# Kernel tuning notes

Measured on AMD Instinct MI355X. Metric: run time of the kernel, lower is better.

Reference implementation:

```python
import jax, jax.numpy as jnp
import numpy as np

N = 100000
E = 1600000
IN_C = 128
OUT_C = 128
EPS = 1e-12  # F.normalize eps


def setup_inputs() -> dict:
    key = jax.random.key(0)
    ks = jax.random.split(key, 8)
    glorot = lambda k, fi, fo: jax.random.uniform(k, (fo, fi), jnp.float32, -1.0, 1.0) * np.sqrt(1.0 / fi)
    return {
        "x": jax.random.normal(ks[0], (N, IN_C), jnp.float32),
        "edge_index": jax.random.randint(ks[1], (2, E), 0, N, jnp.int64),
        "W_l1": glorot(ks[2], IN_C, OUT_C),
        "b_l1": jnp.zeros((OUT_C,), jnp.float32),
        "W_r1": glorot(ks[3], IN_C, OUT_C),
        "W_l2": glorot(ks[4], OUT_C, OUT_C),
        "b_l2": jnp.zeros((OUT_C,), jnp.float32),
        "W_r2": glorot(ks[5], OUT_C, OUT_C),
    }


def _sage_conv(x, src, dst, W_l, b_l, W_r):
    # mean aggregation of source-node features into destination nodes
    deg = jax.ops.segment_sum(jnp.ones((src.shape[0],), x.dtype), dst, num_segments=N)
    agg = jax.ops.segment_sum(x[src], dst, num_segments=N)  # [N, C] scatter-add of gathered features
    agg = agg / jnp.maximum(deg, 1.0)[:, None]
    out = agg @ W_l.T + b_l + x @ W_r.T
    # L2 normalize (F.normalize, p=2, eps=1e-12)
    nrm = jnp.linalg.norm(out, axis=-1, keepdims=True)
    return out / jnp.maximum(nrm, EPS)


def reference(x, edge_index, W_l1, b_l1, W_r1, W_l2, b_l2, W_r2):
    src, dst = edge_index[0], edge_index[1]
    h = _sage_conv(x, src, dst, W_l1, b_l1, W_r1)
    h = _sage_conv(h, src, dst, W_l2, b_l2, W_r2)
    return h
```

## Files before the change

### kernel.cpp

```cpp
#include <hip/hip_runtime.h>
#include <hip/hip_bf16.h>


#define BCAP 16384

typedef __attribute__((ext_vector_type(8))) short bf16x8;
typedef __attribute__((ext_vector_type(4))) float f32x4;

__device__ __forceinline__ ushort f2bf(float f) {
    uint u = __float_as_uint(f);
    uint r = (u + 0x7FFFu + ((u >> 16) & 1u)) >> 16;
    return (ushort)r;
}
__device__ __forceinline__ float bflo(uint u) { return __uint_as_float(u << 16); }
__device__ __forceinline__ float bfhi(uint u) { return __uint_as_float(u & 0xFFFF0000u); }

__global__ void detect_kernel(const int* __restrict__ ei, int* __restrict__ flag) {
    if (threadIdx.x == 0 && blockIdx.x == 0) {
        int z = 1;
        for (int j = 0; j < 64; ++j)
            if (ei[2 * j + 1] != 0) { z = 0; break; }
        *flag = z;
    }
}

__device__ __forceinline__ int load_idx(const void* ei, int is64, size_t i) {
    return is64 ? (int)((const long long*)ei)[i] : ((const int*)ei)[i];
}

__global__ __launch_bounds__(256) void bin_scatter_kernel(
    const void* __restrict__ ei, const int* __restrict__ flagp,
    int* __restrict__ bcursor, uint* __restrict__ pairbuf, int E, int ntiles) {
    __shared__ int cnt[256], pos[256];
    const int tid = threadIdx.x;
    const int is64 = *flagp;
    for (int tile = blockIdx.x; tile < ntiles; tile += gridDim.x) {
        const int base = tile * 2048;
        cnt[tid] = 0;
        __syncthreads();
        int eb[8];
        uint ep[8];
#pragma unroll
        for (int j = 0; j < 8; ++j) {
            const int i = base + tid * 8 + j;
            if (i < E) {
                const int s = load_idx(ei, is64, (size_t)i);
                const int d = load_idx(ei, is64, (size_t)E + i);
                eb[j] = d >> 9;
                ep[j] = ((uint)(d & 511) << 17) | (uint)s;
                atomicAdd(&cnt[eb[j]], 1);
            } else {
                eb[j] = -1;
            }
        }
        __syncthreads();
        pos[tid] = atomicAdd(&bcursor[tid], cnt[tid]);
        __syncthreads();
#pragma unroll
        for (int j = 0; j < 8; ++j) {
            if (eb[j] >= 0) {
                const int p = atomicAdd(&pos[eb[j]], 1);
                if (p < BCAP) pairbuf[(size_t)eb[j] * BCAP + p] = ep[j];
            }
        }
    }
}

__global__ void bucket_scan_kernel(const int* __restrict__ bcount,
                                   int* __restrict__ bbase,
                                   int* __restrict__ rs, int N) {
    __shared__ int wt[4];
    const int tid = threadIdx.x, lane = tid & 63, wid = tid >> 6;
    const int v = bcount[tid];
    int incl = v;
    for (int d = 1; d < 64; d <<= 1) {
        int up = __shfl_up(incl, d, 64);
        if (lane >= d) incl += up;
    }
    if (lane == 63) wt[wid] = incl;
    __syncthreads();
    int woff = 0;
    for (int w = 0; w < wid; ++w) woff += wt[w];
    bbase[tid] = woff + incl - v;
    if (tid == 255) rs[N] = woff + incl;
}

__global__ __launch_bounds__(256) void bucket_degscan_kernel(
    const uint* __restrict__ pairbuf, const int* __restrict__ bcount,
    const int* __restrict__ bbase,
    int* __restrict__ rs, float* __restrict__ invd, int N) {
    __shared__ int dg[512];
    __shared__ int wt[4];
    const int tid = threadIdx.x, lane = tid & 63, wid = tid >> 6, wg = blockIdx.x;
    dg[tid] = 0;
    dg[tid + 256] = 0;
    __syncthreads();
    const int s = wg * BCAP, e = s + bcount[wg];
    for (int i = s + tid; i < e; i += 256)
        atomicAdd(&dg[pairbuf[i] >> 17], 1);
    __syncthreads();
    const int d0 = dg[2 * tid], d1 = dg[2 * tid + 1];
    const int v = d0 + d1;
    int incl = v;
    for (int d = 1; d < 64; d <<= 1) {
        int up = __shfl_up(incl, d, 64);
        if (lane >= d) incl += up;
    }
    if (lane == 63) wt[wid] = incl;
    __syncthreads();
    int woff = 0;
    for (int w = 0; w < wid; ++w) woff += wt[w];
    const int excl = woff + incl - v + bbase[wg];
    const int node = wg * 512 + 2 * tid;
    if (node < N) {
        rs[node] = excl;
        invd[node] = 1.0f / (float)(d0 > 1 ? d0 : 1);
    }
    if (node + 1 < N) {
        rs[node + 1] = excl + d0;
        invd[node + 1] = 1.0f / (float)(d1 > 1 ? d1 : 1);
    }
}

__global__ __launch_bounds__(256) void bucket_fill_kernel(
    const uint* __restrict__ pairbuf, const int* __restrict__ bcount,
    const int* __restrict__ rs, int* __restrict__ csr, int N) {
    __shared__ int cur[512];
    const int tid = threadIdx.x, wg = blockIdx.x;
#pragma unroll
    for (int t = tid; t < 512; t += 256) {
        const int node = wg * 512 + t;
        cur[t] = (node < N) ? rs[node] : 0;
    }
    __syncthreads();
    const int s = wg * BCAP, e = s + bcount[wg];
    for (int i = s + tid; i < e; i += 256) {
        const uint p = pairbuf[i];
        const int pos = atomicAdd(&cur[p >> 17], 1);
        csr[pos] = (int)(p & 0x1FFFFu);
    }
}

__global__ void pack_w_kernel(const float* __restrict__ Wl1, const float* __restrict__ Wr1,
                              const float* __restrict__ Wl2, const float* __restrict__ Wr2,
                              ushort* __restrict__ Wp) {
    const int gtid = blockIdx.x * 256 + threadIdx.x;
    if (gtid >= 8192) return;
    const int layer = gtid >> 12;
    const int c16   = gtid & 4095;
    const int s     = c16 >> 10;
    const int t     = (c16 >> 6) & 15;
    const int lane  = c16 & 63;
    const int c     = t * 16 + (lane & 15);
    const int kbase = s * 32 + (lane >> 4) * 8;
    const float* Wl = layer ? Wl2 : Wl1;
    const float* Wr = layer ? Wr2 : Wr1;
    const float* src = (c < 128) ? (Wl + c * 128 + kbase) : (Wr + (c - 128) * 128 + kbase);
    ushort* dst = Wp + (size_t)layer * 32768 + (size_t)c16 * 8;
#pragma unroll
    for (int j = 0; j < 8; ++j) dst[j] = f2bf(src[j]);
}

template <int AF32>
__global__ __launch_bounds__(256) void sage_mfma_gemm(
    const void* __restrict__ Av, const ushort* __restrict__ Wp,
    unsigned char* __restrict__ ylq, float* __restrict__ scales,
    ushort* __restrict__ yr, int n) {
    __shared__ ushort Wlds[16384];
    const int h = blockIdx.x & 1;
    const int mt = blockIdx.x >> 1;
    for (int i = threadIdx.x; i < 2048; i += 256) {
        const int e = i >> 6, l = i & 63;
        const int ge = (e >> 3) * 16 + h * 8 + (e & 7);
        *(bf16x8*)&Wlds[(size_t)i * 8] = *(const bf16x8*)&Wp[(size_t)(ge * 64 + l) * 8];
    }
    __syncthreads();

    const int wid = threadIdx.x >> 6, lane = threadIdx.x & 63;
    const int koff = (lane >> 4) * 8;
    const int rsub = lane & 15;

    bf16x8 a_cur[4];
    {
        int arow = mt * 64 + wid * 16 + rsub;
        if (arow >= n) arow = 0;
        if (AF32) {
            const float* ap = (const float*)Av + ((size_t)arow << 7) + koff;
#pragma unroll
            for (int s = 0; s < 4; ++s) {
                const float4 f0 = *(const float4*)(ap + s * 32);
                const float4 f1 = *(const float4*)(ap + s * 32 + 4);
                bf16x8 rr;
                rr[0] = (short)f2bf(f0.x); rr[1] = (short)f2bf(f0.y);
                rr[2] = (short)f2bf(f0.z); rr[3] = (short)f2bf(f0.w);
                rr[4] = (short)f2bf(f1.x); rr[5] = (short)f2bf(f1.y);
                rr[6] = (short)f2bf(f1.z); rr[7] = (short)f2bf(f1.w);
                a_cur[s] = rr;
            }
        } else {
            const ushort* ap = (const ushort*)Av + ((size_t)arow << 7) + koff;
#pragma unroll
            for (int s = 0; s < 4; ++s) a_cur[s] = *(const bf16x8*)(ap + s * 32);
        }
    }

    f32x4 acc[8];
    const f32x4 zero = {0.f, 0.f, 0.f, 0.f};
#pragma unroll
    for (int t = 0; t < 8; ++t) acc[t] = zero;

#pragma unroll
    for (int s = 0; s < 4; ++s) {
        const bf16x8 as = a_cur[s];
#pragma unroll
        for (int t = 0; t < 8; ++t) {
            const bf16x8 b = *(const bf16x8*)&Wlds[(size_t)((s * 8 + t) * 64 + lane) * 8];
            acc[t] = __builtin_amdgcn_mfma_f32_16x16x32_bf16(as, b, acc[t], 0, 0, 0);
        }
    }

    const int rowb = mt * 64 + wid * 16 + (lane >> 4) * 4;

    if (h == 0) {
        float mrow[4], invq[4];
#pragma unroll
        for (int rr = 0; rr < 4; ++rr) {
            float m = 0.f;
#pragma unroll
            for (int t = 0; t < 8; ++t) m = fmaxf(m, fabsf(acc[t][rr]));
            m = fmaxf(m, __shfl_xor(m, 1, 64));
            m = fmaxf(m, __shfl_xor(m, 2, 64));
            m = fmaxf(m, __shfl_xor(m, 4, 64));
            m = fmaxf(m, __shfl_xor(m, 8, 64));
            mrow[rr] = m;
            invq[rr] = 127.0f / fmaxf(m, 1e-20f);
        }
        if (rsub == 0) {
#pragma unroll
            for (int rr = 0; rr < 4; ++rr)
                if (rowb + rr < n) scales[rowb + rr] = mrow[rr] * (1.0f / 127.0f);
        }
#pragma unroll
        for (int t = 0; t < 8; ++t) {
            const int col = t * 16 + rsub;
#pragma unroll
            for (int rr = 0; rr < 4; ++rr) {
                const int row = rowb + rr;
                if (row < n) {
                    const int qv = __float2int_rn(acc[t][rr] * invq[rr]) + 128;
                    ylq[((size_t)row << 7) + col] = (unsigned char)qv;
                }
            }
        }
    } else {
#pragma unroll
        for (int t = 0; t < 8; ++t) {
            const int col = t * 16 + rsub;
#pragma unroll
            for (int rr = 0; rr < 4; ++rr) {
                const int row = rowb + rr;
                if (row < n) yr[((size_t)row << 7) + col] = f2bf(acc[t][rr]);
            }
        }
    }
}

template <int OUTF32>
__global__ __launch_bounds__(256) void aggregate_norm_kernel(
    const unsigned char* __restrict__ ylq, const float* __restrict__ scales,
    const ushort* __restrict__ yr, const float* __restrict__ bias,
    const int* __restrict__ csr, const int* __restrict__ rs,
    const float* __restrict__ invd, void* __restrict__ outp, int n) {
    const int wid = threadIdx.x >> 6, lane = threadIdx.x & 63;
    const int g = lane >> 4, t = lane & 15;
    const int node = blockIdx.x * 16 + wid * 4 + g;
    if (node >= n) return;
    const int s = rs[node], e = rs[node + 1];

    float ax[8];
#pragma unroll
    for (int j = 0; j < 8; ++j) ax[j] = 0.f;
    float sumS = 0.f;

    auto acc_row = [&](uint2 u, float sc) {
        sumS += sc;
        ax[0] = fmaf((float)(u.x & 0xffu),         sc, ax[0]);
        ax[1] = fmaf((float)((u.x >> 8) & 0xffu),  sc, ax[1]);
        ax[2] = fmaf((float)((u.x >> 16) & 0xffu), sc, ax[2]);
        ax[3] = fmaf((float)(u.x >> 24),           sc, ax[3]);
        ax[4] = fmaf((float)(u.y & 0xffu),         sc, ax[4]);
        ax[5] = fmaf((float)((u.y >> 8) & 0xffu),  sc, ax[5]);
        ax[6] = fmaf((float)((u.y >> 16) & 0xffu), sc, ax[6]);
        ax[7] = fmaf((float)(u.y >> 24),           sc, ax[7]);
    };

    int q = s;
    while (q < e && (q & 3)) {
        const int c = csr[q++];
        acc_row(*(const uint2*)(ylq + ((size_t)c << 7) + 8 * t), scales[c]);
    }
    for (; q + 4 <= e; q += 4) {
        const int4 c4 = *(const int4*)(csr + q);
        const float s0 = scales[c4.x], s1 = scales[c4.y];
        const float s2 = scales[c4.z], s3 = scales[c4.w];
        const uint2 u0 = *(const uint2*)(ylq + ((size_t)c4.x << 7) + 8 * t);
        const uint2 u1 = *(const uint2*)(ylq + ((size_t)c4.y << 7) + 8 * t);
        const uint2 u2 = *(const uint2*)(ylq + ((size_t)c4.z << 7) + 8 * t);
        const uint2 u3 = *(const uint2*)(ylq + ((size_t)c4.w << 7) + 8 * t);
        acc_row(u0, s0); acc_row(u1, s1); acc_row(u2, s2); acc_row(u3, s3);
    }
    for (; q < e; ++q) {
        const int c = csr[q];
        acc_row(*(const uint2*)(ylq + ((size_t)c << 7) + 8 * t), scales[c]);
    }

    const float iv = invd[node];
    const float base = -128.0f * sumS;
    const uint4 ur = *(const uint4*)(yr + ((size_t)node << 7) + 8 * t);
    const float4 b0 = *(const float4*)(bias + 8 * t);
    const float4 b1 = *(const float4*)(bias + 8 * t + 4);
    float v[8];
    v[0] = fmaf(ax[0] + base, iv, bflo(ur.x) + b0.x);
    v[1] = fmaf(ax[1] + base, iv, bfhi(ur.x) + b0.y);
    v[2] = fmaf(ax[2] + base, iv, bflo(ur.y) + b0.z);
    v[3] = fmaf(ax[3] + base, iv, bfhi(ur.y) + b0.w);
    v[4] = fmaf(ax[4] + base, iv, bflo(ur.z) + b1.x);
    v[5] = fmaf(ax[5] + base, iv, bfhi(ur.z) + b1.y);
    v[6] = fmaf(ax[6] + base, iv, bflo(ur.w) + b1.z);
    v[7] = fmaf(ax[7] + base, iv, bfhi(ur.w) + b1.w);

    float ss = 0.f;
#pragma unroll
    for (int j = 0; j < 8; ++j) ss = fmaf(v[j], v[j], ss);
    ss += __shfl_xor(ss, 1, 64);
    ss += __shfl_xor(ss, 2, 64);
    ss += __shfl_xor(ss, 4, 64);
    ss += __shfl_xor(ss, 8, 64);
    const float sc = 1.0f / fmaxf(sqrtf(ss), 1e-12f);

    if (OUTF32) {
        float4 o0 = {v[0] * sc, v[1] * sc, v[2] * sc, v[3] * sc};
        float4 o1 = {v[4] * sc, v[5] * sc, v[6] * sc, v[7] * sc};
        ((float4*)outp)[((size_t)node << 5) + 2 * t]     = o0;
        ((float4*)outp)[((size_t)node << 5) + 2 * t + 1] = o1;
    } else {
        uint4 o;
        o.x = (uint)f2bf(v[0] * sc) | ((uint)f2bf(v[1] * sc) << 16);
        o.y = (uint)f2bf(v[2] * sc) | ((uint)f2bf(v[3] * sc) << 16);
        o.z = (uint)f2bf(v[4] * sc) | ((uint)f2bf(v[5] * sc) << 16);
        o.w = (uint)f2bf(v[6] * sc) | ((uint)f2bf(v[7] * sc) << 16);
        ((uint4*)outp)[((size_t)node << 4) + t] = o;
    }
}

extern "C" void kernel_launch(void* const* d_in, const int* in_sizes, int n_in,
                              void* d_out, int out_size, void* d_ws, size_t ws_size,
                              hipStream_t stream) {
    const float* x   = (const float*)d_in[0];
    const void*  ei  = d_in[1];
    const float* Wl1 = (const float*)d_in[2];
    const float* bl1 = (const float*)d_in[3];
    const float* Wr1 = (const float*)d_in[4];
    const float* Wl2 = (const float*)d_in[5];
    const float* bl2 = (const float*)d_in[6];
    const float* Wr2 = (const float*)d_in[7];
    float* out = (float*)d_out;

    const int N = in_sizes[0] / 128;
    const int E = in_sizes[1] / 2;

    char* wsb = (char*)d_ws;
    size_t off = 0;
    auto alloc = [&](size_t bytes) -> void* {
        void* p = (void*)(wsb + off);
        off += bytes;
        off = (off + 255) & ~(size_t)255;
        return p;
    };

    int*    rs      = (int*)alloc(4 * (size_t)(N + 1));
    float*  invd    = (float*)alloc(4 * (size_t)N);
    float*  scales  = (float*)alloc(4 * (size_t)N);
    int*    flag    = (int*)alloc(256);
    int*    bcursor = (int*)alloc(4 * 256);
    int*    bbase   = (int*)alloc(4 * 256);
    int*    csr     = (int*)alloc(4 * (size_t)E);
    ushort* h1      = (ushort*)alloc((size_t)N * 128 * 2);
    unsigned char* ylq = (unsigned char*)alloc((size_t)N * 128);
    ushort* yr      = (ushort*)alloc((size_t)N * 128 * 2);
    ushort* Wp      = (ushort*)alloc(2 * 32768 * 2);
    uint*   pairbuf = (uint*)yr;

    const int ab = (N + 15) / 16;
    const int mtiles = (N + 63) / 64;
    const int ntiles = (E + 2047) / 2048;

    detect_kernel<<<1, 64, 0, stream>>>((const int*)ei, flag);
    hipMemsetAsync(bcursor, 0, 4 * 256, stream);
    bin_scatter_kernel<<<512, 256, 0, stream>>>(ei, flag, bcursor, pairbuf, E, ntiles);
    bucket_scan_kernel<<<1, 256, 0, stream>>>(bcursor, bbase, rs, N);
    bucket_degscan_kernel<<<256, 256, 0, stream>>>(pairbuf, bcursor, bbase, rs, invd, N);
    bucket_fill_kernel<<<256, 256, 0, stream>>>(pairbuf, bcursor, rs, csr, N);

    pack_w_kernel<<<32, 256, 0, stream>>>(Wl1, Wr1, Wl2, Wr2, Wp);

    sage_mfma_gemm<1><<<2 * mtiles, 256, 0, stream>>>(x, Wp, ylq, scales, yr, N);
    aggregate_norm_kernel<0><<<ab, 256, 0, stream>>>(ylq, scales, yr, bl1, csr, rs, invd, h1, N);

    sage_mfma_gemm<0><<<2 * mtiles, 256, 0, stream>>>(h1, Wp + 32768, ylq, scales, yr, N);
    aggregate_norm_kernel<1><<<ab, 256, 0, stream>>>(ylq, scales, yr, bl2, csr, rs, invd, out, N);
}
```

Measured before the change: 208.1 us.

## Quantize root projection to int8 and fuse CSR degree-scan with fill

```diff
diff --git a/kernel.cpp b/kernel.cpp
--- a/kernel.cpp
+++ b/kernel.cpp
@@ -85,11 +85,12 @@
     if (tid == 255) rs[N] = woff + incl;
 }
 
-__global__ __launch_bounds__(256) void bucket_degscan_kernel(
+__global__ __launch_bounds__(256) void bucket_build_kernel(
     const uint* __restrict__ pairbuf, const int* __restrict__ bcount,
     const int* __restrict__ bbase,
-    int* __restrict__ rs, float* __restrict__ invd, int N) {
+    int* __restrict__ rs, float* __restrict__ invd, int* __restrict__ csr, int N) {
     __shared__ int dg[512];
+    __shared__ int cur[512];
     __shared__ int wt[4];
     const int tid = threadIdx.x, lane = tid & 63, wid = tid >> 6, wg = blockIdx.x;
     dg[tid] = 0;
@@ -120,20 +121,9 @@
         rs[node + 1] = excl + d0;
         invd[node + 1] = 1.0f / (float)(d1 > 1 ? d1 : 1);
     }
-}
-
-__global__ __launch_bounds__(256) void bucket_fill_kernel(
-    const uint* __restrict__ pairbuf, const int* __restrict__ bcount,
-    const int* __restrict__ rs, int* __restrict__ csr, int N) {
-    __shared__ int cur[512];
-    const int tid = threadIdx.x, wg = blockIdx.x;
-#pragma unroll
-    for (int t = tid; t < 512; t += 256) {
-        const int node = wg * 512 + t;
-        cur[t] = (node < N) ? rs[node] : 0;
-    }
-    __syncthreads();
-    const int s = wg * BCAP, e = s + bcount[wg];
+    cur[2 * tid] = excl;
+    cur[2 * tid + 1] = excl + d0;
+    __syncthreads();
     for (int i = s + tid; i < e; i += 256) {
         const uint p = pairbuf[i];
         const int pos = atomicAdd(&cur[p >> 17], 1);
@@ -165,7 +155,7 @@
 __global__ __launch_bounds__(256) void sage_mfma_gemm(
     const void* __restrict__ Av, const ushort* __restrict__ Wp,
     unsigned char* __restrict__ ylq, float* __restrict__ scales,
-    ushort* __restrict__ yr, int n) {
+    unsigned char* __restrict__ yrq, float* __restrict__ scales_r, int n) {
     __shared__ ushort Wlds[16384];
     const int h = blockIdx.x & 1;
     const int mt = blockIdx.x >> 1;
@@ -220,46 +210,36 @@
     }
 
     const int rowb = mt * 64 + wid * 16 + (lane >> 4) * 4;
-
-    if (h == 0) {
-        float mrow[4], invq[4];
+    unsigned char* dq = h ? yrq : ylq;
+    float* ds = h ? scales_r : scales;
+
+    float mrow[4], invq[4];
+#pragma unroll
+    for (int rr = 0; rr < 4; ++rr) {
+        float m = 0.f;
+#pragma unroll
+        for (int t = 0; t < 8; ++t) m = fmaxf(m, fabsf(acc[t][rr]));
+        m = fmaxf(m, __shfl_xor(m, 1, 64));
+        m = fmaxf(m, __shfl_xor(m, 2, 64));
+        m = fmaxf(m, __shfl_xor(m, 4, 64));
+        m = fmaxf(m, __shfl_xor(m, 8, 64));
+        mrow[rr] = m;
+        invq[rr] = 127.0f / fmaxf(m, 1e-20f);
+    }
+    if (rsub == 0) {
+#pragma unroll
+        for (int rr = 0; rr < 4; ++rr)
+            if (rowb + rr < n) ds[rowb + rr] = mrow[rr] * (1.0f / 127.0f);
+    }
+#pragma unroll
+    for (int t = 0; t < 8; ++t) {
+        const int col = t * 16 + rsub;
 #pragma unroll
         for (int rr = 0; rr < 4; ++rr) {
-            float m = 0.f;
-#pragma unroll
-            for (int t = 0; t < 8; ++t) m = fmaxf(m, fabsf(acc[t][rr]));
-            m = fmaxf(m, __shfl_xor(m, 1, 64));
-            m = fmaxf(m, __shfl_xor(m, 2, 64));
-            m = fmaxf(m, __shfl_xor(m, 4, 64));
-            m = fmaxf(m, __shfl_xor(m, 8, 64));
-            mrow[rr] = m;
-            invq[rr] = 127.0f / fmaxf(m, 1e-20f);
-        }
-        if (rsub == 0) {
-#pragma unroll
-            for (int rr = 0; rr < 4; ++rr)
-                if (rowb + rr < n) scales[rowb + rr] = mrow[rr] * (1.0f / 127.0f);
-        }
-#pragma unroll
-        for (int t = 0; t < 8; ++t) {
-            const int col = t * 16 + rsub;
-#pragma unroll
-            for (int rr = 0; rr < 4; ++rr) {
-                const int row = rowb + rr;
-                if (row < n) {
-                    const int qv = __float2int_rn(acc[t][rr] * invq[rr]) + 128;
-                    ylq[((size_t)row << 7) + col] = (unsigned char)qv;
-                }
-            }
-        }
-    } else {
-#pragma unroll
-        for (int t = 0; t < 8; ++t) {
-            const int col = t * 16 + rsub;
-#pragma unroll
-            for (int rr = 0; rr < 4; ++rr) {
-                const int row = rowb + rr;
-                if (row < n) yr[((size_t)row << 7) + col] = f2bf(acc[t][rr]);
+            const int row = rowb + rr;
+            if (row < n) {
+                const int qv = __float2int_rn(acc[t][rr] * invq[rr]) + 128;
+                dq[((size_t)row << 7) + col] = (unsigned char)qv;
             }
         }
     }
@@ -268,9 +248,10 @@
 template <int OUTF32>
 __global__ __launch_bounds__(256) void aggregate_norm_kernel(
     const unsigned char* __restrict__ ylq, const float* __restrict__ scales,
-    const ushort* __restrict__ yr, const float* __restrict__ bias,
-    const int* __restrict__ csr, const int* __restrict__ rs,
-    const float* __restrict__ invd, void* __restrict__ outp, int n) {
+    const unsigned char* __restrict__ yrq, const float* __restrict__ scales_r,
+    const float* __restrict__ bias, const int* __restrict__ csr,
+    const int* __restrict__ rs, const float* __restrict__ invd,
+    void* __restrict__ outp, int n) {
     const int wid = threadIdx.x >> 6, lane = threadIdx.x & 63;
     const int g = lane >> 4, t = lane & 15;
     const int node = blockIdx.x * 16 + wid * 4 + g;
@@ -316,18 +297,28 @@
 
     const float iv = invd[node];
     const float base = -128.0f * sumS;
-    const uint4 ur = *(const uint4*)(yr + ((size_t)node << 7) + 8 * t);
+    const float sr = scales_r[node];
+    const uint2 ur = *(const uint2*)(yrq + ((size_t)node << 7) + 8 * t);
     const float4 b0 = *(const float4*)(bias + 8 * t);
     const float4 b1 = *(const float4*)(bias + 8 * t + 4);
+    float yv[8];
+    yv[0] = ((float)(ur.x & 0xffu)         - 128.0f) * sr;
+    yv[1] = ((float)((ur.x >> 8) & 0xffu)  - 128.0f) * sr;
+    yv[2] = ((float)((ur.x >> 16) & 0xffu) - 128.0f) * sr;
+    yv[3] = ((float)(ur.x >> 24)           - 128.0f) * sr;
+    yv[4] = ((float)(ur.y & 0xffu)         - 128.0f) * sr;
+    yv[5] = ((float)((ur.y >> 8) & 0xffu)  - 128.0f) * sr;
+    yv[6] = ((float)((ur.y >> 16) & 0xffu) - 128.0f) * sr;
+    yv[7] = ((float)(ur.y >> 24)           - 128.0f) * sr;
     float v[8];
-    v[0] = fmaf(ax[0] + base, iv, bflo(ur.x) + b0.x);
-    v[1] = fmaf(ax[1] + base, iv, bfhi(ur.x) + b0.y);
-    v[2] = fmaf(ax[2] + base, iv, bflo(ur.y) + b0.z);
-    v[3] = fmaf(ax[3] + base, iv, bfhi(ur.y) + b0.w);
-    v[4] = fmaf(ax[4] + base, iv, bflo(ur.z) + b1.x);
-    v[5] = fmaf(ax[5] + base, iv, bfhi(ur.z) + b1.y);
-    v[6] = fmaf(ax[6] + base, iv, bflo(ur.w) + b1.z);
-    v[7] = fmaf(ax[7] + base, iv, bfhi(ur.w) + b1.w);
+    v[0] = fmaf(ax[0] + base, iv, yv[0] + b0.x);
+    v[1] = fmaf(ax[1] + base, iv, yv[1] + b0.y);
+    v[2] = fmaf(ax[2] + base, iv, yv[2] + b0.z);
+    v[3] = fmaf(ax[3] + base, iv, yv[3] + b0.w);
+    v[4] = fmaf(ax[4] + base, iv, yv[4] + b1.x);
+    v[5] = fmaf(ax[5] + base, iv, yv[5] + b1.y);
+    v[6] = fmaf(ax[6] + base, iv, yv[6] + b1.z);
+    v[7] = fmaf(ax[7] + base, iv, yv[7] + b1.w);
 
     float ss = 0.f;
 #pragma unroll
@@ -378,18 +369,19 @@
         return p;
     };
 
-    int*    rs      = (int*)alloc(4 * (size_t)(N + 1));
-    float*  invd    = (float*)alloc(4 * (size_t)N);
-    float*  scales  = (float*)alloc(4 * (size_t)N);
-    int*    flag    = (int*)alloc(256);
-    int*    bcursor = (int*)alloc(4 * 256);
-    int*    bbase   = (int*)alloc(4 * 256);
-    int*    csr     = (int*)alloc(4 * (size_t)E);
-    ushort* h1      = (ushort*)alloc((size_t)N * 128 * 2);
+    int*    rs       = (int*)alloc(4 * (size_t)(N + 1));
+    float*  invd     = (float*)alloc(4 * (size_t)N);
+    float*  scales   = (float*)alloc(4 * (size_t)N);
+    float*  scales_r = (float*)alloc(4 * (size_t)N);
+    int*    flag     = (int*)alloc(256);
+    int*    bcursor  = (int*)alloc(4 * 256);
+    int*    bbase    = (int*)alloc(4 * 256);
+    int*    csr      = (int*)alloc(4 * (size_t)E);
+    ushort* h1       = (ushort*)alloc((size_t)N * 128 * 2);
     unsigned char* ylq = (unsigned char*)alloc((size_t)N * 128);
-    ushort* yr      = (ushort*)alloc((size_t)N * 128 * 2);
-    ushort* Wp      = (ushort*)alloc(2 * 32768 * 2);
-    uint*   pairbuf = (uint*)yr;
+    unsigned char* yrq = (unsigned char*)alloc((size_t)N * 128);
+    ushort* Wp       = (ushort*)alloc(2 * 32768 * 2);
+    uint*   pairbuf  = (uint*)h1;
 
     const int ab = (N + 15) / 16;
     const int mtiles = (N + 63) / 64;
@@ -399,14 +391,13 @@
     hipMemsetAsync(bcursor, 0, 4 * 256, stream);
     bin_scatter_kernel<<<512, 256, 0, stream>>>(ei, flag, bcursor, pairbuf, E, ntiles);
     bucket_scan_kernel<<<1, 256, 0, stream>>>(bcursor, bbase, rs, N);
-    bucket_degscan_kernel<<<256, 256, 0, stream>>>(pairbuf, bcursor, bbase, rs, invd, N);
-    bucket_fill_kernel<<<256, 256, 0, stream>>>(pairbuf, bcursor, rs, csr, N);
+    bucket_build_kernel<<<256, 256, 0, stream>>>(pairbuf, bcursor, bbase, rs, invd, csr, N);
 
     pack_w_kernel<<<32, 256, 0, stream>>>(Wl1, Wr1, Wl2, Wr2, Wp);
 
-    sage_mfma_gemm<1><<<2 * mtiles, 256, 0, stream>>>(x, Wp, ylq, scales, yr, N);
-    aggregate_norm_kernel<0><<<ab, 256, 0, stream>>>(ylq, scales, yr, bl1, csr, rs, invd, h1, N);
-
-    sage_mfma_gemm<0><<<2 * mtiles, 256, 0, stream>>>(h1, Wp + 32768, ylq, scales, yr, N);
-    aggregate_norm_kernel<1><<<ab, 256, 0, stream>>>(ylq, scales, yr, bl2, csr, rs, invd, out, N);
-}
+    sage_mfma_gemm<1><<<2 * mtiles, 256, 0, stream>>>(x, Wp, ylq, scales, yrq, scales_r, N);
+    aggregate_norm_kernel<0><<<ab, 256, 0, stream>>>(ylq, scales, yrq, scales_r, bl1, csr, rs, invd, h1, N);
+
+    sage_mfma_gemm<0><<<2 * mtiles, 256, 0, stream>>>(h1, Wp + 32768, ylq, scales, yrq, scales_r, N);
+    aggregate_norm_kernel<1><<<ab, 256, 0, stream>>>(ylq, scales, yrq, scales_r, bl2, csr, rs, invd, out, N);
+}
```

New measurement: 207.1 us. No clear change (-0.5%).
